# Performance work log

Measured on AMD Instinct MI355X. Metric: run time of the kernel, lower is better.

Reference implementation:

```python
import jax, jax.numpy as jnp
import numpy as np

B, T, C = 4, 2048, 1024
E = 8            # n_expert
K = 2            # n_expert_per_token
H = 1408         # moe_intermediate_size
HS = 1408 * 2    # shared expert intermediate (moe_intermediate_size * n_shared_expert)


def setup_inputs() -> dict:
    key = jax.random.key(0)
    k = jax.random.split(key, 8)
    s = 0.02
    return {
        "x":   jax.random.normal(k[0], (B, T, C), jnp.float32),
        "Wg":  jax.random.normal(k[1], (C, E), jnp.float32) * s,      # router gate
        "W1":  jax.random.normal(k[2], (E, C, H), jnp.float32) * s,   # fc_1 per expert
        "W2":  jax.random.normal(k[3], (E, C, H), jnp.float32) * s,   # fc_2 per expert
        "W3":  jax.random.normal(k[4], (E, H, C), jnp.float32) * s,   # proj per expert
        "Ws1": jax.random.normal(k[5], (C, HS), jnp.float32) * s,     # shared fc_1
        "Ws2": jax.random.normal(k[6], (C, HS), jnp.float32) * s,     # shared fc_2
        "Ws3": jax.random.normal(k[7], (HS, C), jnp.float32) * s,     # shared proj
    }


def reference(x, Wg, W1, W2, W3, Ws1, Ws2, Ws3):
    b, t, c = x.shape
    xf = x.reshape(-1, c)                       # [N, C]
    n = xf.shape[0]

    # Router: top-k then softmax over the selected logits (float32 softmax).
    router = xf @ Wg                            # [N, E]
    top_logits, idx = jax.lax.top_k(router, K)  # [N, K]
    probs = jax.nn.softmax(top_logits.astype(jnp.float32), axis=-1).astype(x.dtype)

    # token_expert_weights: scatter probs into dense [N, E] per-expert weights.
    w = jnp.zeros((n, E), x.dtype).at[jnp.arange(n)[:, None], idx].add(probs)

    # Per-expert gated MLP on all tokens; zero-weight tokens contribute nothing,
    # matching the masked gather/scatter-add of the original.
    h = jax.nn.silu(jnp.einsum('tc,ech->eth', xf, W1)) * jnp.einsum('tc,ech->eth', xf, W2)
    y = jnp.einsum('eth,ehc,te->tc', h, W3, w)  # weighted combine
    y = y.reshape(b, t, c)

    # Shared expert on the residual input.
    hs = jax.nn.silu(xf @ Ws1) * (xf @ Ws2)     # [N, HS]
    y = y + (hs @ Ws3).reshape(b, t, c)
    return y
```

## Files before the change

### kernel.cpp

```cpp
#include <hip/hip_runtime.h>
#include <cstdint>

#define NTOK 8192
#define CDIM 1024
#define HDIM 1408
#define HSDIM 2816
#define NEXP 8

typedef __attribute__((ext_vector_type(8))) short s8v;
typedef __attribute__((ext_vector_type(4))) float f4v;
typedef __attribute__((ext_vector_type(8))) unsigned short u16x8;

__device__ __forceinline__ unsigned short f2bf(float f) {
    unsigned int u = __float_as_uint(f);
    unsigned int r = (u + 0x7fffu + ((u >> 16) & 1u)) >> 16;
    return (unsigned short)r;
}
__device__ __forceinline__ float bf2f(unsigned short u) {
    return __uint_as_float(((unsigned int)u) << 16);
}

__device__ __forceinline__ void gld_lds16(const unsigned short* g, unsigned short* l) {
    __builtin_amdgcn_global_load_lds(
        (const __attribute__((address_space(1))) void*)g,
        (__attribute__((address_space(3))) void*)l, 16, 0, 0);
}


__global__ void cvt_bf16_kernel(const float4* __restrict__ in, ushort4* __restrict__ out, int n4) {
    int i = blockIdx.x * blockDim.x + threadIdx.x;
    if (i < n4) {
        float4 v = in[i];
        ushort4 o;
        o.x = f2bf(v.x); o.y = f2bf(v.y); o.z = f2bf(v.z); o.w = f2bf(v.w);
        out[i] = o;
    }
}

__global__ __launch_bounds__(256) void transpose_cvt_kernel(
    const float* __restrict__ in0, const float* __restrict__ in1,
    unsigned short* __restrict__ out0, unsigned short* __restrict__ out1,
    int R, int Cc, int zsplit) {
    __shared__ float T[64][68];
    int z = blockIdx.z;
    const float* in = (z < zsplit) ? in0 : in1;
    unsigned short* out = (z < zsplit) ? out0 : out1;
    int zz = (z < zsplit) ? z : z - zsplit;
    const size_t bs = (size_t)R * Cc;
    in += zz * bs; out += zz * bs;

    const int t = threadIdx.x;
    const int r0 = blockIdx.y * 64, c0 = blockIdx.x * 64;

    {
        const int rl = t >> 2, cq = t & 3;
        const float* src = in + (size_t)(r0 + rl) * Cc + c0;
#pragma unroll
        for (int i = 0; i < 4; i++) {
            float4 v = *(const float4*)(src + (cq + 4 * i) * 4);
            *(float4*)&T[rl][(cq + 4 * i) * 4] = v;
        }
    }
    __syncthreads();
    {
        const int cl = t >> 2, rq = t & 3;
        unsigned short* dst = out + (size_t)(c0 + cl) * R + r0 + rq * 16;
        u16x8 lo, hi;
#pragma unroll
        for (int j = 0; j < 8; j++) lo[j] = f2bf(T[rq * 16 + j][cl]);
#pragma unroll
        for (int j = 0; j < 8; j++) hi[j] = f2bf(T[rq * 16 + 8 + j][cl]);
        *(u16x8*)dst = lo;
        *(u16x8*)(dst + 8) = hi;
    }
}

__global__ void router_kernel(const float* __restrict__ x, const float* __restrict__ Wg,
                              int* __restrict__ idxK, float* __restrict__ probK,
                              int* __restrict__ meta) {
    int t = blockIdx.x;
    int lane = threadIdx.x;
    const float* xr = x + (size_t)t * CDIM;
    float acc[NEXP];
#pragma unroll
    for (int e = 0; e < NEXP; e++) acc[e] = 0.f;
    for (int c = lane; c < CDIM; c += 64) {
        float xv = xr[c];
        const float* wr = Wg + c * NEXP;
#pragma unroll
        for (int e = 0; e < NEXP; e++) acc[e] += xv * wr[e];
    }
#pragma unroll
    for (int e = 0; e < NEXP; e++)
        for (int off = 32; off > 0; off >>= 1)
            acc[e] += __shfl_down(acc[e], off, 64);
    if (lane == 0) {
        int b0 = 0; float v0 = acc[0];
#pragma unroll
        for (int e = 1; e < NEXP; e++) if (acc[e] > v0) { v0 = acc[e]; b0 = e; }
        int b1 = -1; float v1 = -1e30f;
#pragma unroll
        for (int e = 0; e < NEXP; e++) if (e != b0 && acc[e] > v1) { v1 = acc[e]; b1 = e; }
        float p0 = 1.f / (1.f + __expf(v1 - v0));
        idxK[2 * t] = b0; idxK[2 * t + 1] = b1;
        probK[2 * t] = p0; probK[2 * t + 1] = 1.f - p0;
        atomicAdd(&meta[b0], 1);
        atomicAdd(&meta[b1], 1);
    }
}

__global__ void offsets_kernel(int* meta) {
    int s = 0;
    for (int e = 0; e < NEXP; e++) { meta[8 + e] = s; meta[16 + e] = s; s += meta[e]; }
}

__global__ void fill_kernel(const int* __restrict__ idxK, const float* __restrict__ probK,
                            int* __restrict__ meta, int* __restrict__ rowT, float* __restrict__ rowW,
                            int* __restrict__ tokSlot) {
    int t = blockIdx.x * 256 + threadIdx.x;
    if (t >= NTOK) return;
#pragma unroll
    for (int k = 0; k < 2; k++) {
        int e = idxK[2 * t + k];
        int p = atomicAdd(&meta[16 + e], 1);
        rowT[p] = t;
        rowW[p] = probK[2 * t + k];
        tokSlot[2 * t + k] = p;
    }
}

__global__ __launch_bounds__(256) void gemm12_kernel(
    const unsigned short* __restrict__ xb,
    const unsigned short* __restrict__ w1, const unsigned short* __restrict__ w2,
    const unsigned short* __restrict__ ws1, const unsigned short* __restrict__ ws2,
    unsigned short* __restrict__ hE, unsigned short* __restrict__ hS,
    const int* __restrict__ rowT, const int* __restrict__ meta) {
    const int id = blockIdx.x;
    int z, m0, n0; bool SH;
    if (id < 3520) { SH = false; z = id & 7; int q = id >> 3; m0 = (q % 20) * 128; n0 = (q / 20) * 64; }
    else           { SH = true;  z = 8; int q = id - 3520; m0 = (q & 63) * 128; n0 = (q >> 6) * 64; }
    const int M = SH ? NTOK : meta[z];
    const int base = SH ? 0 : meta[8 + z];
    if (m0 >= M) return;

    const unsigned short* B1 = SH ? ws1 : w1 + (size_t)z * HDIM * CDIM;
    const unsigned short* B2 = SH ? ws2 : w2 + (size_t)z * HDIM * CDIM;

    __shared__ unsigned short L[16384];

    const int tid = threadIdx.x;
    const int srow = tid >> 2;
    const int key = (tid >> 3) & 3;
    const int co = ((tid & 3) ^ key) << 3;

    int am0 = m0 + srow;       am0 = am0 < M ? am0 : M - 1;
    int am1 = m0 + 64 + srow;  am1 = am1 < M ? am1 : M - 1;
    long ar0 = SH ? am0 : rowT[base + am0];
    long ar1 = SH ? am1 : rowT[base + am1];
    const unsigned short* a0p = xb + (size_t)ar0 * CDIM + co;
    const unsigned short* a1p = xb + (size_t)ar1 * CDIM + co;
    const unsigned short* b1p = B1 + (size_t)(n0 + srow) * CDIM + co;
    const unsigned short* b2p = B2 + (size_t)(n0 + srow) * CDIM + co;

    const int w = tid >> 6, lane = tid & 63;
    const int wm = (w >> 1) * 64, wn = (w & 1) * 32;
    const int quad = lane >> 4, l15 = lane & 15;
    const int rcx = (quad ^ ((l15 >> 1) & 3)) << 3;

    f4v acc1[4][2], acc2[4][2];
#pragma unroll
    for (int i = 0; i < 4; i++)
#pragma unroll
        for (int j = 0; j < 2; j++) {
            f4v zz = {0.f, 0.f, 0.f, 0.f};
            acc1[i][j] = zz; acc2[i][j] = zz;
        }

#define STAGE12(b, k0) do { \
        gld_lds16(a0p + (k0), L + (b) * 4096 + tid * 8); \
        gld_lds16(a1p + (k0), L + (b) * 4096 + 2048 + tid * 8); \
        gld_lds16(b1p + (k0), L + 8192 + (b) * 2048 + tid * 8); \
        gld_lds16(b2p + (k0), L + 12288 + (b) * 2048 + tid * 8); } while (0)

    auto compute = [&](int b) {
        const unsigned short* Ab = L + b * 4096;
        const unsigned short* B1b = L + 8192 + b * 2048;
        const unsigned short* B2b = L + 12288 + b * 2048;
        s8v af[4], bf1[2], bf2[2];
#pragma unroll
        for (int mt = 0; mt < 4; mt++)
            af[mt] = *(const s8v*)(Ab + (wm + mt * 16 + l15) * 32 + rcx);
#pragma unroll
        for (int nt = 0; nt < 2; nt++) {
            bf1[nt] = *(const s8v*)(B1b + (wn + nt * 16 + l15) * 32 + rcx);
            bf2[nt] = *(const s8v*)(B2b + (wn + nt * 16 + l15) * 32 + rcx);
        }
#pragma unroll
        for (int mt = 0; mt < 4; mt++)
#pragma unroll
            for (int nt = 0; nt < 2; nt++) {
                acc1[mt][nt] = __builtin_amdgcn_mfma_f32_16x16x32_bf16(af[mt], bf1[nt], acc1[mt][nt], 0, 0, 0);
                acc2[mt][nt] = __builtin_amdgcn_mfma_f32_16x16x32_bf16(af[mt], bf2[nt], acc2[mt][nt], 0, 0, 0);
            }
    };

    const int NS = CDIM / 32;
    STAGE12(0, 0);
    __syncthreads();
#pragma unroll 1
    for (int ks = 0; ks < NS; ks++) {
        if (ks + 1 < NS) STAGE12((ks + 1) & 1, (ks + 1) * 32);
        compute(ks & 1);
        __syncthreads();
    }
#undef STAGE12

#pragma unroll
    for (int mt = 0; mt < 4; mt++) {
#pragma unroll
        for (int r = 0; r < 4; r++) {
            int gm = m0 + wm + mt * 16 + quad * 4 + r;
            if (gm < M) {
                unsigned short* hrow = SH ? hS + (size_t)gm * HSDIM
                                          : hE + (size_t)(base + gm) * HDIM;
#pragma unroll
                for (int nt = 0; nt < 2; nt++) {
                    float z1 = acc1[mt][nt][r];
                    float z2 = acc2[mt][nt][r];
                    float hv = (z1 / (1.f + __expf(-z1))) * z2;
                    hrow[n0 + wn + nt * 16 + l15] = f2bf(hv);
                }
            }
        }
    }
}

__global__ __launch_bounds__(256) void gemm3_kernel(
    const unsigned short* __restrict__ hE, const unsigned short* __restrict__ hS,
    const unsigned short* __restrict__ w3, const unsigned short* __restrict__ ws3,
    float* __restrict__ Out, unsigned short* __restrict__ pE,
    const int* __restrict__ rowT, const float* __restrict__ rowW, const int* __restrict__ meta) {
    const int id = blockIdx.x;
    int z, m0, n0; bool SH;
    if (id < 1280) { SH = false; z = id & 7; int q = id >> 3; m0 = (q % 20) * 128; n0 = (q / 20) * 128; }
    else           { SH = true;  z = 8; int q = id - 1280; m0 = (q & 63) * 128; n0 = (q >> 6) * 128; }
    const int M = SH ? NTOK : meta[z];
    const int base = SH ? 0 : meta[8 + z];
    if (m0 >= M) return;
    const int K = SH ? HSDIM : HDIM;
    const unsigned short* A = SH ? hS : hE;
    const unsigned short* B = SH ? ws3 : w3 + (size_t)z * CDIM * HDIM;

    __shared__ unsigned short L[16384];

    const int tid = threadIdx.x;
    const int srow = tid >> 2;
    const int key = (tid >> 3) & 3;
    const int co = ((tid & 3) ^ key) << 3;

    int am0 = m0 + srow;       am0 = am0 < M ? am0 : M - 1;
    int am1 = m0 + 64 + srow;  am1 = am1 < M ? am1 : M - 1;
    const unsigned short* a0p = A + (size_t)(base + am0) * K + co;
    const unsigned short* a1p = A + (size_t)(base + am1) * K + co;
    const unsigned short* b0p = B + (size_t)(n0 + srow) * K + co;
    const unsigned short* b1p = B + (size_t)(n0 + 64 + srow) * K + co;

    const int w = tid >> 6, lane = tid & 63;
    const int wm = (w >> 1) * 64, wn = (w & 1) * 64;
    const int quad = lane >> 4, l15 = lane & 15;
    const int rcx = (quad ^ ((l15 >> 1) & 3)) << 3;

    f4v acc[4][4];
#pragma unroll
    for (int i = 0; i < 4; i++)
#pragma unroll
        for (int j = 0; j < 4; j++) {
            f4v zz = {0.f, 0.f, 0.f, 0.f};
            acc[i][j] = zz;
        }

#define STAGE3(b, k0) do { \
        gld_lds16(a0p + (k0), L + (b) * 4096 + tid * 8); \
        gld_lds16(a1p + (k0), L + (b) * 4096 + 2048 + tid * 8); \
        gld_lds16(b0p + (k0), L + 8192 + (b) * 4096 + tid * 8); \
        gld_lds16(b1p + (k0), L + 8192 + (b) * 4096 + 2048 + tid * 8); } while (0)

    auto compute = [&](int b) {
        const unsigned short* Ab = L + b * 4096;
        const unsigned short* Bb = L + 8192 + b * 4096;
        s8v af[4], bf[4];
#pragma unroll
        for (int mt = 0; mt < 4; mt++)
            af[mt] = *(const s8v*)(Ab + (wm + mt * 16 + l15) * 32 + rcx);
#pragma unroll
        for (int nt = 0; nt < 4; nt++)
            bf[nt] = *(const s8v*)(Bb + (wn + nt * 16 + l15) * 32 + rcx);
#pragma unroll
        for (int mt = 0; mt < 4; mt++)
#pragma unroll
            for (int nt = 0; nt < 4; nt++)
                acc[mt][nt] = __builtin_amdgcn_mfma_f32_16x16x32_bf16(af[mt], bf[nt], acc[mt][nt], 0, 0, 0);
    };

    const int NS = K / 32;
    STAGE3(0, 0);
    __syncthreads();
#pragma unroll 1
    for (int ks = 0; ks < NS; ks++) {
        if (ks + 1 < NS) STAGE3((ks + 1) & 1, (ks + 1) * 32);
        compute(ks & 1);
        __syncthreads();
    }
#undef STAGE3

#pragma unroll
    for (int mt = 0; mt < 4; mt++) {
#pragma unroll
        for (int r = 0; r < 4; r++) {
            int gm = m0 + wm + mt * 16 + quad * 4 + r;
            if (gm < M) {
                if (SH) {
                    size_t o = (size_t)gm * CDIM + n0 + wn + l15;
#pragma unroll
                    for (int nt = 0; nt < 4; nt++)
                        Out[o + nt * 16] = acc[mt][nt][r];
                } else {
                    size_t o = (size_t)(base + gm) * CDIM + n0 + wn + l15;
#pragma unroll
                    for (int nt = 0; nt < 4; nt++)
                        pE[o + nt * 16] = f2bf(acc[mt][nt][r]);
                }
            }
        }
    }
}

__global__ __launch_bounds__(256) void combine_kernel(
    float* __restrict__ Out, const unsigned short* __restrict__ pE,
    const int* __restrict__ tokSlot, const float* __restrict__ rowW) {
    const int t = blockIdx.x;
    const int c = threadIdx.x * 4;
    const int s0 = tokSlot[2 * t], s1 = tokSlot[2 * t + 1];
    const float w0 = rowW[s0], w1 = rowW[s1];
    float* op = Out + (size_t)t * CDIM + c;
    float4 o = *(float4*)op;
    ushort4 a = *(const ushort4*)(pE + (size_t)s0 * CDIM + c);
    ushort4 b = *(const ushort4*)(pE + (size_t)s1 * CDIM + c);
    o.x += w0 * bf2f(a.x) + w1 * bf2f(b.x);
    o.y += w0 * bf2f(a.y) + w1 * bf2f(b.y);
    o.z += w0 * bf2f(a.z) + w1 * bf2f(b.z);
    o.w += w0 * bf2f(a.w) + w1 * bf2f(b.w);
    *(float4*)op = o;
}


extern "C" void kernel_launch(void* const* d_in, const int* in_sizes, int n_in,
                              void* d_out, int out_size, void* d_ws, size_t ws_size,
                              hipStream_t stream) {
    const float* x   = (const float*)d_in[0];
    const float* Wg  = (const float*)d_in[1];
    const float* W1  = (const float*)d_in[2];
    const float* W2  = (const float*)d_in[3];
    const float* W3  = (const float*)d_in[4];
    const float* Ws1 = (const float*)d_in[5];
    const float* Ws2 = (const float*)d_in[6];
    const float* Ws3 = (const float*)d_in[7];
    float* out = (float*)d_out;

    char* p = (char*)d_ws;
    auto carve = [&](size_t bytes) {
        char* r = p;
        p += (bytes + 255) & ~(size_t)255;
        return r;
    };
    unsigned short* xb   = (unsigned short*)carve((size_t)NTOK * CDIM * 2);
    unsigned short* w1t  = (unsigned short*)carve((size_t)NEXP * HDIM * CDIM * 2);
    unsigned short* w2t  = (unsigned short*)carve((size_t)NEXP * HDIM * CDIM * 2);
    unsigned short* w3t  = (unsigned short*)carve((size_t)NEXP * CDIM * HDIM * 2);
    unsigned short* ws1t = (unsigned short*)carve((size_t)HSDIM * CDIM * 2);
    unsigned short* ws2t = (unsigned short*)carve((size_t)HSDIM * CDIM * 2);
    unsigned short* ws3t = (unsigned short*)carve((size_t)CDIM * HSDIM * 2);
    unsigned short* hE   = (unsigned short*)carve((size_t)2 * NTOK * HDIM * 2);
    unsigned short* hS   = (unsigned short*)carve((size_t)NTOK * HSDIM * 2);
    int*   idxK   = (int*)carve((size_t)NTOK * 2 * 4);
    float* probK  = (float*)carve((size_t)NTOK * 2 * 4);
    int*   rowT   = (int*)carve((size_t)2 * NTOK * 4);
    float* rowW   = (float*)carve((size_t)2 * NTOK * 4);
    int*   tokSlot= (int*)carve((size_t)2 * NTOK * 4);
    int*   meta   = (int*)carve(256);

    unsigned short* pE = w1t;

    cvt_bf16_kernel<<<(NTOK * CDIM / 4 + 255) / 256, 256, 0, stream>>>(
        (const float4*)x, (ushort4*)xb, NTOK * CDIM / 4);
    transpose_cvt_kernel<<<dim3(HDIM / 64, CDIM / 64, 16), 256, 0, stream>>>(
        W1, W2, w1t, w2t, CDIM, HDIM, 8);
    transpose_cvt_kernel<<<dim3(CDIM / 64, HDIM / 64, 8), 256, 0, stream>>>(
        W3, W3, w3t, w3t, HDIM, CDIM, 8);
    transpose_cvt_kernel<<<dim3(HSDIM / 64, CDIM / 64, 2), 256, 0, stream>>>(
        Ws1, Ws2, ws1t, ws2t, CDIM, HSDIM, 1);
    transpose_cvt_kernel<<<dim3(CDIM / 64, HSDIM / 64, 1), 256, 0, stream>>>(
        Ws3, Ws3, ws3t, ws3t, HSDIM, CDIM, 1);

    hipMemsetAsync(meta, 0, 256, stream);
    router_kernel<<<NTOK, 64, 0, stream>>>(x, Wg, idxK, probK, meta);
    offsets_kernel<<<1, 1, 0, stream>>>(meta);
    fill_kernel<<<NTOK / 256, 256, 0, stream>>>(idxK, probK, meta, rowT, rowW, tokSlot);

    gemm12_kernel<<<3520 + 2816, 256, 0, stream>>>(
        xb, w1t, w2t, ws1t, ws2t, hE, hS, rowT, meta);
    gemm3_kernel<<<1280 + 512, 256, 0, stream>>>(
        hE, hS, w3t, ws3t, out, pE, rowT, rowW, meta);
    combine_kernel<<<NTOK, 256, 0, stream>>>(out, pE, tokSlot, rowW);
}
```

Before: 869.8 us.

## Restructure gated GEMM12 into 8-wave 256-row tiles with interleaved LDS pipeline

The fused fc1/fc2 GEMM kernel now uses 512 threads, 256x64 output tiles and a K step of 64 instead of 32. Global-to-LDS loads are split into sub-stages and interleaved with MFMA phases, with explicit vmcnt waits, s_barrier and s_setprio, so loads overlap compute. The larger tile reuses each weight tile across more rows and halves the number of K iterations. In exchange it uses much more LDS (96KB), which lowers occupancy, and it wastes more work on padded rows for small experts.

After: 876.1 us. Within noise of the previous version (+0.7%).

```diff
diff --git a/kernel.cpp b/kernel.cpp
--- a/kernel.cpp
+++ b/kernel.cpp
@@ -129,7 +129,7 @@
     }
 }
 
-__global__ __launch_bounds__(256) void gemm12_kernel(
+__global__ __launch_bounds__(512) void gemm12_kernel(
     const unsigned short* __restrict__ xb,
     const unsigned short* __restrict__ w1, const unsigned short* __restrict__ w2,
     const unsigned short* __restrict__ ws1, const unsigned short* __restrict__ ws2,
@@ -137,8 +137,8 @@
     const int* __restrict__ rowT, const int* __restrict__ meta) {
     const int id = blockIdx.x;
     int z, m0, n0; bool SH;
-    if (id < 3520) { SH = false; z = id & 7; int q = id >> 3; m0 = (q % 20) * 128; n0 = (q / 20) * 64; }
-    else           { SH = true;  z = 8; int q = id - 3520; m0 = (q & 63) * 128; n0 = (q >> 6) * 64; }
+    if (id < 1760) { SH = false; z = id & 7; int q = id >> 3; m0 = (q % 10) * 256; n0 = (q / 10) * 64; }
+    else           { SH = true;  z = 8; int q = id - 1760; m0 = (q & 31) * 256; n0 = (q >> 5) * 64; }
     const int M = SH ? NTOK : meta[z];
     const int base = SH ? 0 : meta[8 + z];
     if (m0 >= M) return;
@@ -146,26 +146,37 @@
     const unsigned short* B1 = SH ? ws1 : w1 + (size_t)z * HDIM * CDIM;
     const unsigned short* B2 = SH ? ws2 : w2 + (size_t)z * HDIM * CDIM;
 
-    __shared__ unsigned short L[16384];
+    __shared__ unsigned short L[49152];
 
     const int tid = threadIdx.x;
-    const int srow = tid >> 2;
-    const int key = (tid >> 3) & 3;
-    const int co = ((tid & 3) ^ key) << 3;
-
-    int am0 = m0 + srow;       am0 = am0 < M ? am0 : M - 1;
-    int am1 = m0 + 64 + srow;  am1 = am1 < M ? am1 : M - 1;
-    long ar0 = SH ? am0 : rowT[base + am0];
-    long ar1 = SH ? am1 : rowT[base + am1];
-    const unsigned short* a0p = xb + (size_t)ar0 * CDIM + co;
-    const unsigned short* a1p = xb + (size_t)ar1 * CDIM + co;
-    const unsigned short* b1p = B1 + (size_t)(n0 + srow) * CDIM + co;
-    const unsigned short* b2p = B2 + (size_t)(n0 + srow) * CDIM + co;
+    const int trow = tid >> 3;
+    const int colg = ((tid & 7) ^ (trow & 7)) << 3;
+
+    int r0 = m0 + trow, r1 = m0 + 64 + trow, r2 = m0 + 128 + trow, r3 = m0 + 192 + trow;
+    r0 = r0 < M ? r0 : M - 1; r1 = r1 < M ? r1 : M - 1;
+    r2 = r2 < M ? r2 : M - 1; r3 = r3 < M ? r3 : M - 1;
+    const int g0 = SH ? r0 : rowT[base + r0];
+    const int g1 = SH ? r1 : rowT[base + r1];
+    const int g2 = SH ? r2 : rowT[base + r2];
+    const int g3 = SH ? r3 : rowT[base + r3];
+    const unsigned short* gA0 = xb + (size_t)g0 * CDIM + colg;
+    const unsigned short* gA1 = xb + (size_t)g1 * CDIM + colg;
+    const unsigned short* gA2 = xb + (size_t)g2 * CDIM + colg;
+    const unsigned short* gA3 = xb + (size_t)g3 * CDIM + colg;
+    const unsigned short* gB1 = B1 + (size_t)(n0 + trow) * CDIM + colg;
+    const unsigned short* gB2 = B2 + (size_t)(n0 + trow) * CDIM + colg;
 
     const int w = tid >> 6, lane = tid & 63;
-    const int wm = (w >> 1) * 64, wn = (w & 1) * 32;
+    const int wq = w >> 1;
+    const int wn = (w & 1) * 32;
     const int quad = lane >> 4, l15 = lane & 15;
-    const int rcx = (quad ^ ((l15 >> 1) & 3)) << 3;
+    const int kxor = l15 & 7;
+    int cX[2];
+    cX[0] = (quad ^ kxor) << 3;
+    cX[1] = ((4 + quad) ^ kxor) << 3;
+    int roA[2], roB[2];
+    roA[0] = (wq * 32 + l15) * 64; roA[1] = roA[0] + 16 * 64;
+    roB[0] = (wn + l15) * 64;      roB[1] = roB[0] + 16 * 64;
 
     f4v acc1[4][2], acc2[4][2];
 #pragma unroll
@@ -176,63 +187,109 @@
             acc1[i][j] = zz; acc2[i][j] = zz;
         }
 
-#define STAGE12(b, k0) do { \
-        gld_lds16(a0p + (k0), L + (b) * 4096 + tid * 8); \
-        gld_lds16(a1p + (k0), L + (b) * 4096 + 2048 + tid * 8); \
-        gld_lds16(b1p + (k0), L + 8192 + (b) * 2048 + tid * 8); \
-        gld_lds16(b2p + (k0), L + 12288 + (b) * 2048 + tid * 8); } while (0)
-
-    auto compute = [&](int b) {
-        const unsigned short* Ab = L + b * 4096;
-        const unsigned short* B1b = L + 8192 + b * 2048;
-        const unsigned short* B2b = L + 12288 + b * 2048;
-        s8v af[4], bf1[2], bf2[2];
-#pragma unroll
-        for (int mt = 0; mt < 4; mt++)
-            af[mt] = *(const s8v*)(Ab + (wm + mt * 16 + l15) * 32 + rcx);
-#pragma unroll
-        for (int nt = 0; nt < 2; nt++) {
-            bf1[nt] = *(const s8v*)(B1b + (wn + nt * 16 + l15) * 32 + rcx);
-            bf2[nt] = *(const s8v*)(B2b + (wn + nt * 16 + l15) * 32 + rcx);
-        }
-#pragma unroll
-        for (int mt = 0; mt < 4; mt++)
+    s8v bq1[2][2], bq2[2][2], af[2][2];
+
+    auto ST_A0 = [&](int s, int t) {
+        gld_lds16(gA0 + (size_t)t * 64, L + s * 24576 + tid * 8);
+        gld_lds16(gA1 + (size_t)t * 64, L + s * 24576 + 4096 + tid * 8);
+    };
+    auto ST_A1 = [&](int s, int t) {
+        gld_lds16(gA2 + (size_t)t * 64, L + s * 24576 + 8192 + tid * 8);
+        gld_lds16(gA3 + (size_t)t * 64, L + s * 24576 + 12288 + tid * 8);
+    };
+    auto ST_B = [&](int s, int t) {
+        gld_lds16(gB1 + (size_t)t * 64, L + s * 24576 + 16384 + tid * 8);
+        gld_lds16(gB2 + (size_t)t * 64, L + s * 24576 + 20480 + tid * 8);
+    };
+    auto READB = [&](int s) {
+        const unsigned short* B1s = L + s * 24576 + 16384;
+        const unsigned short* B2s = L + s * 24576 + 20480;
+#pragma unroll
+        for (int q = 0; q < 2; q++)
 #pragma unroll
             for (int nt = 0; nt < 2; nt++) {
-                acc1[mt][nt] = __builtin_amdgcn_mfma_f32_16x16x32_bf16(af[mt], bf1[nt], acc1[mt][nt], 0, 0, 0);
-                acc2[mt][nt] = __builtin_amdgcn_mfma_f32_16x16x32_bf16(af[mt], bf2[nt], acc2[mt][nt], 0, 0, 0);
+                bq1[q][nt] = *(const s8v*)(B1s + roB[nt] + cX[q]);
+                bq2[q][nt] = *(const s8v*)(B2s + roB[nt] + cX[q]);
             }
     };
-
-    const int NS = CDIM / 32;
-    STAGE12(0, 0);
-    __syncthreads();
+    auto READA = [&](int s, int h) {
+        const unsigned short* As = L + s * 24576 + h * 8192;
+#pragma unroll
+        for (int q = 0; q < 2; q++)
+#pragma unroll
+            for (int mt = 0; mt < 2; mt++)
+                af[q][mt] = *(const s8v*)(As + roA[mt] + cX[q]);
+    };
+    auto MFMA16 = [&](int h) {
+#pragma unroll
+        for (int q = 0; q < 2; q++)
+#pragma unroll
+            for (int mt = 0; mt < 2; mt++)
+#pragma unroll
+                for (int nt = 0; nt < 2; nt++) {
+                    acc1[h * 2 + mt][nt] = __builtin_amdgcn_mfma_f32_16x16x32_bf16(
+                        af[q][mt], bq1[q][nt], acc1[h * 2 + mt][nt], 0, 0, 0);
+                    acc2[h * 2 + mt][nt] = __builtin_amdgcn_mfma_f32_16x16x32_bf16(
+                        af[q][mt], bq2[q][nt], acc2[h * 2 + mt][nt], 0, 0, 0);
+                }
+    };
+
+    ST_A0(0, 0); ST_A1(0, 0); ST_B(0, 0); ST_A0(1, 1);
+    asm volatile("s_waitcnt vmcnt(2)");
+    __builtin_amdgcn_sched_barrier(0);
+    __builtin_amdgcn_s_barrier();
+
 #pragma unroll 1
-    for (int ks = 0; ks < NS; ks++) {
-        if (ks + 1 < NS) STAGE12((ks + 1) & 1, (ks + 1) * 32);
-        compute(ks & 1);
-        __syncthreads();
-    }
-#undef STAGE12
-
-#pragma unroll
-    for (int mt = 0; mt < 4; mt++) {
-#pragma unroll
-        for (int r = 0; r < 4; r++) {
-            int gm = m0 + wm + mt * 16 + quad * 4 + r;
-            if (gm < M) {
-                unsigned short* hrow = SH ? hS + (size_t)gm * HSDIM
-                                          : hE + (size_t)(base + gm) * HDIM;
-#pragma unroll
-                for (int nt = 0; nt < 2; nt++) {
-                    float z1 = acc1[mt][nt][r];
-                    float z2 = acc2[mt][nt][r];
-                    float hv = (z1 / (1.f + __expf(-z1))) * z2;
-                    hrow[n0 + wn + nt * 16 + l15] = f2bf(hv);
+    for (int i = 0; i < 8; i++) {
+        const int t1 = 2 * i + 1;
+        const int t2 = (2 * i + 2 < 16) ? 2 * i + 2 : 15;
+        const int t3 = (2 * i + 3 < 16) ? 2 * i + 3 : 15;
+        READB(0); READA(0, 0);
+        ST_A1(1, t1);
+        __builtin_amdgcn_s_barrier();
+        __builtin_amdgcn_s_setprio(1); MFMA16(0); __builtin_amdgcn_s_setprio(0);
+        __builtin_amdgcn_s_barrier();
+        READA(0, 1);
+        ST_B(1, t1); ST_A0(0, t2);
+        __builtin_amdgcn_s_barrier();
+        __builtin_amdgcn_s_setprio(1); MFMA16(1); __builtin_amdgcn_s_setprio(0);
+        asm volatile("s_waitcnt vmcnt(2)");
+        __builtin_amdgcn_sched_barrier(0);
+        __builtin_amdgcn_s_barrier();
+        READB(1); READA(1, 0);
+        ST_A1(0, t2); ST_B(0, t2);
+        __builtin_amdgcn_s_barrier();
+        __builtin_amdgcn_s_setprio(1); MFMA16(0); __builtin_amdgcn_s_setprio(0);
+        __builtin_amdgcn_s_barrier();
+        READA(1, 1);
+        ST_A0(1, t3);
+        __builtin_amdgcn_s_barrier();
+        __builtin_amdgcn_s_setprio(1); MFMA16(1); __builtin_amdgcn_s_setprio(0);
+        asm volatile("s_waitcnt vmcnt(2)");
+        __builtin_amdgcn_sched_barrier(0);
+        __builtin_amdgcn_s_barrier();
+    }
+    asm volatile("s_waitcnt vmcnt(0)");
+
+#pragma unroll
+    for (int h = 0; h < 2; h++)
+#pragma unroll
+        for (int mt = 0; mt < 2; mt++)
+#pragma unroll
+            for (int r = 0; r < 4; r++) {
+                int gm = m0 + h * 128 + wq * 32 + mt * 16 + quad * 4 + r;
+                if (gm < M) {
+                    unsigned short* hrow = SH ? hS + (size_t)gm * HSDIM
+                                              : hE + (size_t)(base + gm) * HDIM;
+#pragma unroll
+                    for (int nt = 0; nt < 2; nt++) {
+                        float z1 = acc1[h * 2 + mt][nt][r];
+                        float z2 = acc2[h * 2 + mt][nt][r];
+                        float hv = (z1 / (1.f + __expf(-z1))) * z2;
+                        hrow[n0 + wn + nt * 16 + l15] = f2bf(hv);
+                    }
                 }
             }
-        }
-    }
 }
 
 __global__ __launch_bounds__(256) void gemm3_kernel(
@@ -407,7 +464,7 @@
     offsets_kernel<<<1, 1, 0, stream>>>(meta);
     fill_kernel<<<NTOK / 256, 256, 0, stream>>>(idxK, probK, meta, rowT, rowW, tokSlot);
 
-    gemm12_kernel<<<3520 + 2816, 256, 0, stream>>>(
+    gemm12_kernel<<<1760 + 1408, 512, 0, stream>>>(
         xb, w1t, w2t, ws1t, ws2t, hE, hS, rowT, meta);
     gemm3_kernel<<<1280 + 512, 256, 0, stream>>>(
         hE, hS, w3t, ws3t, out, pE, rowT, rowW, meta);
```

## Fuse router, input conversion and weight transposes into one prep kernel

Applied to the files above, without the earlier changes.

Merges the x bf16 conversion, the four weight transpose-convert launches and the router into a single prep_kernel that dispatches on block index, with the router now handling four tokens per 256-thread block. This removes several launches and the serialization gaps between them, and lets small-grid pieces overlap with the others. Separately, gemm3 now schedules the shared-expert tiles first and the routed-expert tiles after, so the dense work is issued before the variable-size expert tiles, many of which exit early. The fused kernel always reserves LDS for the transpose even in the router and convert branches, which can lower occupancy there.

Result: faster. 826.4 us (-5.0%).

```diff
diff --git a/kernel.cpp b/kernel.cpp
--- a/kernel.cpp
+++ b/kernel.cpp
@@ -27,31 +27,19 @@
 }
 
 
-__global__ void cvt_bf16_kernel(const float4* __restrict__ in, ushort4* __restrict__ out, int n4) {
-    int i = blockIdx.x * blockDim.x + threadIdx.x;
-    if (i < n4) {
-        float4 v = in[i];
-        ushort4 o;
-        o.x = f2bf(v.x); o.y = f2bf(v.y); o.z = f2bf(v.z); o.w = f2bf(v.w);
-        out[i] = o;
-    }
-}
-
-__global__ __launch_bounds__(256) void transpose_cvt_kernel(
-    const float* __restrict__ in0, const float* __restrict__ in1,
-    unsigned short* __restrict__ out0, unsigned short* __restrict__ out1,
-    int R, int Cc, int zsplit) {
-    __shared__ float T[64][68];
-    int z = blockIdx.z;
-    const float* in = (z < zsplit) ? in0 : in1;
-    unsigned short* out = (z < zsplit) ? out0 : out1;
-    int zz = (z < zsplit) ? z : z - zsplit;
-    const size_t bs = (size_t)R * Cc;
-    in += zz * bs; out += zz * bs;
-
+#define P_RTR 2048
+#define P_CVT 8192
+#define P_T1 (22 * 16 * 16)
+#define P_T2 (16 * 22 * 8)
+#define P_T3 (44 * 16 * 2)
+#define P_T4 (16 * 44 * 1)
+#define P_TOTAL (P_RTR + P_CVT + P_T1 + P_T2 + P_T3 + P_T4)
+
+__device__ __forceinline__ void transpose_tile(
+    float (*T)[68], const float* __restrict__ in, unsigned short* __restrict__ out,
+    int R, int Cc, int bx, int by) {
     const int t = threadIdx.x;
-    const int r0 = blockIdx.y * 64, c0 = blockIdx.x * 64;
-
+    const int r0 = by * 64, c0 = bx * 64;
     {
         const int rl = t >> 2, cq = t & 3;
         const float* src = in + (size_t)(r0 + rl) * Cc + c0;
@@ -75,37 +63,90 @@
     }
 }
 
-__global__ void router_kernel(const float* __restrict__ x, const float* __restrict__ Wg,
-                              int* __restrict__ idxK, float* __restrict__ probK,
-                              int* __restrict__ meta) {
-    int t = blockIdx.x;
-    int lane = threadIdx.x;
-    const float* xr = x + (size_t)t * CDIM;
-    float acc[NEXP];
-#pragma unroll
-    for (int e = 0; e < NEXP; e++) acc[e] = 0.f;
-    for (int c = lane; c < CDIM; c += 64) {
-        float xv = xr[c];
-        const float* wr = Wg + c * NEXP;
-#pragma unroll
-        for (int e = 0; e < NEXP; e++) acc[e] += xv * wr[e];
-    }
-#pragma unroll
-    for (int e = 0; e < NEXP; e++)
-        for (int off = 32; off > 0; off >>= 1)
-            acc[e] += __shfl_down(acc[e], off, 64);
-    if (lane == 0) {
-        int b0 = 0; float v0 = acc[0];
-#pragma unroll
-        for (int e = 1; e < NEXP; e++) if (acc[e] > v0) { v0 = acc[e]; b0 = e; }
-        int b1 = -1; float v1 = -1e30f;
-#pragma unroll
-        for (int e = 0; e < NEXP; e++) if (e != b0 && acc[e] > v1) { v1 = acc[e]; b1 = e; }
-        float p0 = 1.f / (1.f + __expf(v1 - v0));
-        idxK[2 * t] = b0; idxK[2 * t + 1] = b1;
-        probK[2 * t] = p0; probK[2 * t + 1] = 1.f - p0;
-        atomicAdd(&meta[b0], 1);
-        atomicAdd(&meta[b1], 1);
+__global__ __launch_bounds__(256) void prep_kernel(
+    const float* __restrict__ x, const float* __restrict__ Wg,
+    const float* __restrict__ W1, const float* __restrict__ W2, const float* __restrict__ W3,
+    const float* __restrict__ Ws1, const float* __restrict__ Ws2, const float* __restrict__ Ws3,
+    unsigned short* __restrict__ xb,
+    unsigned short* __restrict__ w1t, unsigned short* __restrict__ w2t,
+    unsigned short* __restrict__ w3t,
+    unsigned short* __restrict__ ws1t, unsigned short* __restrict__ ws2t,
+    unsigned short* __restrict__ ws3t,
+    int* __restrict__ idxK, float* __restrict__ probK, int* __restrict__ meta) {
+    __shared__ float T[64][68];
+    int bid = blockIdx.x;
+    const int tid = threadIdx.x;
+
+    if (bid < P_RTR) {
+        const int t = bid * 4 + (tid >> 6);
+        const int lane = tid & 63;
+        const float* xr = x + (size_t)t * CDIM;
+        float acc[NEXP];
+#pragma unroll
+        for (int e = 0; e < NEXP; e++) acc[e] = 0.f;
+        for (int c = lane; c < CDIM; c += 64) {
+            float xv = xr[c];
+            const float* wr = Wg + c * NEXP;
+#pragma unroll
+            for (int e = 0; e < NEXP; e++) acc[e] += xv * wr[e];
+        }
+#pragma unroll
+        for (int e = 0; e < NEXP; e++)
+            for (int off = 32; off > 0; off >>= 1)
+                acc[e] += __shfl_down(acc[e], off, 64);
+        if (lane == 0) {
+            int b0 = 0; float v0 = acc[0];
+#pragma unroll
+            for (int e = 1; e < NEXP; e++) if (acc[e] > v0) { v0 = acc[e]; b0 = e; }
+            int b1 = -1; float v1 = -1e30f;
+#pragma unroll
+            for (int e = 0; e < NEXP; e++) if (e != b0 && acc[e] > v1) { v1 = acc[e]; b1 = e; }
+            float p0 = 1.f / (1.f + __expf(v1 - v0));
+            idxK[2 * t] = b0; idxK[2 * t + 1] = b1;
+            probK[2 * t] = p0; probK[2 * t + 1] = 1.f - p0;
+            atomicAdd(&meta[b0], 1);
+            atomicAdd(&meta[b1], 1);
+        }
+        return;
+    }
+    bid -= P_RTR;
+    if (bid < P_CVT) {
+        const int i = bid * 256 + tid;
+        float4 v = ((const float4*)x)[i];
+        ushort4 o;
+        o.x = f2bf(v.x); o.y = f2bf(v.y); o.z = f2bf(v.z); o.w = f2bf(v.w);
+        ((ushort4*)xb)[i] = o;
+        return;
+    }
+    bid -= P_CVT;
+    if (bid < P_T1) {
+        const int bx = bid % 22, by = (bid / 22) % 16, z = bid / (22 * 16);
+        const float* in = (z < 8) ? W1 : W2;
+        unsigned short* out = (z < 8) ? w1t : w2t;
+        const int zz = (z < 8) ? z : z - 8;
+        const size_t bs = (size_t)CDIM * HDIM;
+        transpose_tile(T, in + zz * bs, out + zz * bs, CDIM, HDIM, bx, by);
+        return;
+    }
+    bid -= P_T1;
+    if (bid < P_T2) {
+        const int bx = bid % 16, by = (bid / 16) % 22, z = bid / (16 * 22);
+        const size_t bs = (size_t)HDIM * CDIM;
+        transpose_tile(T, W3 + z * bs, w3t + z * bs, HDIM, CDIM, bx, by);
+        return;
+    }
+    bid -= P_T2;
+    if (bid < P_T3) {
+        const int bx = bid % 44, by = (bid / 44) % 16, z = bid / (44 * 16);
+        const float* in = (z == 0) ? Ws1 : Ws2;
+        unsigned short* out = (z == 0) ? ws1t : ws2t;
+        transpose_tile(T, in, out, CDIM, HSDIM, bx, by);
+        return;
+    }
+    bid -= P_T3;
+    {
+        const int bx = bid % 16, by = bid / 16;
+        transpose_tile(T, Ws3, ws3t, HSDIM, CDIM, bx, by);
     }
 }
 
@@ -242,8 +283,8 @@
     const int* __restrict__ rowT, const float* __restrict__ rowW, const int* __restrict__ meta) {
     const int id = blockIdx.x;
     int z, m0, n0; bool SH;
-    if (id < 1280) { SH = false; z = id & 7; int q = id >> 3; m0 = (q % 20) * 128; n0 = (q / 20) * 128; }
-    else           { SH = true;  z = 8; int q = id - 1280; m0 = (q & 63) * 128; n0 = (q >> 6) * 128; }
+    if (id < 512) { SH = true;  z = 8; int q = id; m0 = (q & 63) * 128; n0 = (q >> 6) * 128; }
+    else          { SH = false; int r = id - 512; z = r & 7; int q = r >> 3; m0 = (q % 20) * 128; n0 = (q / 20) * 128; }
     const int M = SH ? NTOK : meta[z];
     const int base = SH ? 0 : meta[8 + z];
     if (m0 >= M) return;
@@ -391,25 +432,16 @@
 
     unsigned short* pE = w1t;
 
-    cvt_bf16_kernel<<<(NTOK * CDIM / 4 + 255) / 256, 256, 0, stream>>>(
-        (const float4*)x, (ushort4*)xb, NTOK * CDIM / 4);
-    transpose_cvt_kernel<<<dim3(HDIM / 64, CDIM / 64, 16), 256, 0, stream>>>(
-        W1, W2, w1t, w2t, CDIM, HDIM, 8);
-    transpose_cvt_kernel<<<dim3(CDIM / 64, HDIM / 64, 8), 256, 0, stream>>>(
-        W3, W3, w3t, w3t, HDIM, CDIM, 8);
-    transpose_cvt_kernel<<<dim3(HSDIM / 64, CDIM / 64, 2), 256, 0, stream>>>(
-        Ws1, Ws2, ws1t, ws2t, CDIM, HSDIM, 1);
-    transpose_cvt_kernel<<<dim3(CDIM / 64, HSDIM / 64, 1), 256, 0, stream>>>(
-        Ws3, Ws3, ws3t, ws3t, HSDIM, CDIM, 1);
-
     hipMemsetAsync(meta, 0, 256, stream);
-    router_kernel<<<NTOK, 64, 0, stream>>>(x, Wg, idxK, probK, meta);
+    prep_kernel<<<P_TOTAL, 256, 0, stream>>>(
+        x, Wg, W1, W2, W3, Ws1, Ws2, Ws3,
+        xb, w1t, w2t, w3t, ws1t, ws2t, ws3t, idxK, probK, meta);
     offsets_kernel<<<1, 1, 0, stream>>>(meta);
     fill_kernel<<<NTOK / 256, 256, 0, stream>>>(idxK, probK, meta, rowT, rowW, tokSlot);
 
     gemm12_kernel<<<3520 + 2816, 256, 0, stream>>>(
         xb, w1t, w2t, ws1t, ws2t, hE, hS, rowT, meta);
-    gemm3_kernel<<<1280 + 512, 256, 0, stream>>>(
+    gemm3_kernel<<<512 + 1280, 256, 0, stream>>>(
         hE, hS, w3t, ws3t, out, pE, rowT, rowW, meta);
     combine_kernel<<<NTOK, 256, 0, stream>>>(out, pE, tokSlot, rowW);
 }
```
